# Kernel tuning notes

Measured on AMD Instinct MI355X. Metric: run time of the kernel, lower is better.

Reference implementation:

```python
import jax, jax.numpy as jnp
import numpy as np

N_USER, N_ITEM, N_BUNDLE = 200000, 100000, 50000
EMBED_DIM = 128
B, L = 8192, 100  # batch of bundles, max items per bundle


def setup_inputs() -> dict:
    key = jax.random.key(0)
    ks = jax.random.split(key, 12)
    d, d2 = EMBED_DIM, 2 * EMBED_DIM
    x_u = jax.random.randint(ks[0], (B,), 0, N_USER)
    x_b = jax.random.randint(ks[1], (B,), 0, N_BUNDLE)
    items = jax.random.randint(ks[2], (B, L), 0, N_ITEM)
    # ragged bundle sizes in [10, L]; padded+masked form of the CSR gather
    lengths = jax.random.randint(ks[3], (B,), 10, L + 1)
    mask = jnp.arange(L)[None, :] < lengths[:, None]  # [B, L] bool
    return {
        "x_u": x_u,
        "x_b": x_b,
        "items": items,
        "mask": mask,
        "emb_u": jax.random.normal(ks[4], (N_USER, d), jnp.float32) * 0.1,
        "emb_i": jax.random.normal(ks[5], (N_ITEM, d), jnp.float32) * 0.1,
        "emb_b": jax.random.normal(ks[6], (N_BUNDLE, d), jnp.float32) * 0.1,
        "A": jax.random.normal(ks[7], (N_ITEM, d), jnp.float32) * 0.1,
        "fc1_w": jax.random.normal(ks[8], (d2, d2), jnp.float32) / np.sqrt(d2),
        "fc1_b": jnp.zeros((d2,), jnp.float32),
        "fc2_w": jax.random.normal(ks[9], (d2, d2), jnp.float32) / np.sqrt(d2),
        "fc2_b": jnp.zeros((d2,), jnp.float32),
        "out_w": jax.random.normal(ks[10], (1, d2), jnp.float32) / np.sqrt(d2),
        "out_b": jnp.zeros((1,), jnp.float32),
    }


def reference(x_u, x_b, items, mask, emb_u, emb_i, emb_b, A,
              fc1_w, fc1_b, fc2_w, fc2_b, out_w, out_b):
    # DAM.forward_bundle with the attention() per-bundle loop vectorized
    h_u = emb_u[x_u]                       # [B, d]
    h_b = emb_b[x_b]                       # [B, d]
    item_e = emb_i[items]                  # [B, L, d] ragged gather (padded)
    a_e = A[items]                         # [B, L, d]
    # w = softmax_l( sum_d e_u * A[item] ) per bundle, over valid items only
    scores = jnp.einsum('bd,bld->bl', h_u, a_e)
    scores = jnp.where(mask, scores, -jnp.inf)
    w = jax.nn.softmax(scores, axis=1)     # [B, L]
    h_x = jnp.einsum('bl,bld->bd', w, item_e)
    h = jnp.concatenate([h_u, h_b + h_x], axis=1)   # [B, 2d]
    h = jax.nn.leaky_relu(h @ fc1_w.T + fc1_b)
    h = jax.nn.leaky_relu(h @ fc2_w.T + fc2_b)
    return h @ out_w.T + out_b             # [B, 1]
```

## Files before the change

### kernel.cpp

```cpp
#include <hip/hip_runtime.h>
#include <hip/hip_bf16.h>

#define D   128
#define D2  256
#define H1P 272

typedef short bf16x8 __attribute__((ext_vector_type(8)));
typedef float f32x4  __attribute__((ext_vector_type(4)));

__device__ __forceinline__ float bf2f(unsigned short u) {
    return __uint_as_float(((unsigned int)u) << 16);
}
__device__ __forceinline__ float bflo(unsigned int p) { return __uint_as_float(p << 16); }
__device__ __forceinline__ float bfhi(unsigned int p) { return __uint_as_float(p & 0xffff0000u); }
__device__ __forceinline__ unsigned short f2bf(float f) {
    __hip_bfloat16 h = __float2bfloat16(f);
    return *(unsigned short*)&h;
}

template<bool BF>
__device__ __forceinline__ float ld1(const void* p, size_t i) {
    if constexpr (BF) return bf2f(((const unsigned short*)p)[i]);
    else              return ((const float*)p)[i];
}

template<bool BF>
__device__ __forceinline__ void load8f(const void* p, size_t elem_off, float* r) {
    if constexpr (BF) {
        uint4 v = *(const uint4*)((const unsigned short*)p + elem_off);
        r[0]=bflo(v.x); r[1]=bfhi(v.x); r[2]=bflo(v.y); r[3]=bfhi(v.y);
        r[4]=bflo(v.z); r[5]=bfhi(v.z); r[6]=bflo(v.w); r[7]=bfhi(v.w);
    } else {
        const float4* q = (const float4*)((const float*)p + elem_off);
        float4 a = q[0], b = q[1];
        r[0]=a.x; r[1]=a.y; r[2]=a.z; r[3]=a.w;
        r[4]=b.x; r[5]=b.y; r[6]=b.z; r[7]=b.w;
    }
}

__device__ __forceinline__ int probe_bf16(const unsigned int* probe, int lane) {
    int cnt = 0;
    #pragma unroll
    for (int i = 0; i < 4; ++i) {
        unsigned int e = (probe[lane + 64 * i] >> 7) & 0xffu;
        cnt += (e >= 90 && e < 130) ? 1 : 0;
    }
    #pragma unroll
    for (int o = 32; o; o >>= 1) cnt += __shfl_xor(cnt, o);
    return cnt;
}

template<bool BF>
__device__ __forceinline__ void attn_body(
    const int* __restrict__ x_u, const int* __restrict__ x_b,
    const int* __restrict__ items, const void* __restrict__ mask, int mmode,
    const void* __restrict__ emb_u, const void* __restrict__ emb_i,
    const void* __restrict__ emb_b, const void* __restrict__ Aw,
    unsigned short* __restrict__ h_out, int L,
    float* hu_s, float* sc_s, float* w_s, int* it_s,
    int* cnt_s, float* reds_s, float (*part_s)[132])
{
    const int b  = blockIdx.x;
    const int t  = threadIdx.x;
    const int wv = t >> 6, ln = t & 63;

    const int xu = x_u[b], xb = x_b[b];
    float hu = 0.f;
    if (t < D) { hu = ld1<BF>(emb_u, (size_t)xu * D + t); hu_s[t] = hu; }

    bool valid = false;
    if (t < L && t < 128) {
        const size_t mi = (size_t)b * L + t;
        it_s[t] = items[mi];
        if (mmode == 0)      valid = ((const int*)mask)[mi] != 0;
        else if (mmode == 1) valid = ((const unsigned char*)mask)[mi] != 0;
        else                 valid = ((const unsigned short*)mask)[mi] != 0;
    }
    unsigned long long bm = __ballot(valid);
    if (ln == 0) cnt_s[wv] = __popcll(bm);
    __syncthreads();
    const int len = cnt_s[0] + cnt_s[1] + cnt_s[2] + cnt_s[3];

    const int item = t >> 1, half = t & 1;
    if (item < len) {
        float acc = 0.f, r[8];
        const size_t base = (size_t)it_s[item] * D + half * 64;
        const float4* hu4 = (const float4*)hu_s + half * 16;
        #pragma unroll
        for (int c = 0; c < 8; ++c) {
            load8f<BF>(Aw, base + 8 * c, r);
            float4 ha = hu4[2 * c], hb2 = hu4[2 * c + 1];
            acc += ha.x * r[0] + ha.y * r[1] + ha.z * r[2] + ha.w * r[3]
                 + hb2.x * r[4] + hb2.y * r[5] + hb2.z * r[6] + hb2.w * r[7];
        }
        acc += __shfl_xor(acc, 1);
        if (half == 0) sc_s[item] = acc;
    }
    if (t >= len && t < 128) it_s[t] = it_s[0];
    __syncthreads();

    const int g = t >> 4, m16 = t & 15;

    uint4 pre0[4], pre1[4];
    if constexpr (BF) {
        const unsigned short* EI = (const unsigned short*)emb_i;
        #pragma unroll
        for (int i = 0; i < 4; ++i) {
            pre0[i] = *(const uint4*)(EI + (size_t)it_s[32 * i + g]      * D + 8 * m16);
            pre1[i] = *(const uint4*)(EI + (size_t)it_s[32 * i + 16 + g] * D + 8 * m16);
        }
    }

    const float e = (t < len) ? __expf(sc_s[t]) : 0.f;
    if (t < 128) w_s[t] = e;
    float sm = e;
    #pragma unroll
    for (int o = 32; o; o >>= 1) sm += __shfl_xor(sm, o);
    if (ln == 0) reds_s[wv] = sm;
    __syncthreads();
    sm = reds_s[0] + reds_s[1] + reds_s[2] + reds_s[3];
    const float inv = (sm > 0.f) ? 1.f / sm : 0.f;

    float acc8[8];
    #pragma unroll
    for (int k = 0; k < 8; ++k) acc8[k] = 0.f;
    if constexpr (BF) {
        #pragma unroll
        for (int i = 0; i < 4; ++i) {
            const float w0 = w_s[32 * i + g], w1 = w_s[32 * i + 16 + g];
            const uint4 p0 = pre0[i], p1 = pre1[i];
            acc8[0] += w0 * bflo(p0.x) + w1 * bflo(p1.x);
            acc8[1] += w0 * bfhi(p0.x) + w1 * bfhi(p1.x);
            acc8[2] += w0 * bflo(p0.y) + w1 * bflo(p1.y);
            acc8[3] += w0 * bfhi(p0.y) + w1 * bfhi(p1.y);
            acc8[4] += w0 * bflo(p0.z) + w1 * bflo(p1.z);
            acc8[5] += w0 * bfhi(p0.z) + w1 * bfhi(p1.z);
            acc8[6] += w0 * bflo(p0.w) + w1 * bflo(p1.w);
            acc8[7] += w0 * bfhi(p0.w) + w1 * bfhi(p1.w);
        }
    } else {
        const int nit = (len + 31) & ~31;
        for (int i = 0; i < nit; i += 32) {
            const float w0 = w_s[i + g], w1 = w_s[i + 16 + g];
            float r0[8], r1[8];
            load8f<false>(emb_i, (size_t)it_s[i + g] * D + 8 * m16, r0);
            load8f<false>(emb_i, (size_t)it_s[i + 16 + g] * D + 8 * m16, r1);
            #pragma unroll
            for (int k = 0; k < 8; ++k) acc8[k] += w0 * r0[k] + w1 * r1[k];
        }
    }
    f32x4 v0 = {acc8[0] * inv, acc8[1] * inv, acc8[2] * inv, acc8[3] * inv};
    f32x4 v1 = {acc8[4] * inv, acc8[5] * inv, acc8[6] * inv, acc8[7] * inv};
    *(f32x4*)&part_s[g][8 * m16]     = v0;
    *(f32x4*)&part_s[g][8 * m16 + 4] = v1;
    __syncthreads();

    if (t < D) {
        float hx = 0.f;
        #pragma unroll
        for (int gg = 0; gg < 16; ++gg) hx += part_s[gg][t];
        const float hbv = ld1<BF>(emb_b, (size_t)xb * D + t);
        h_out[(size_t)b * D2 + t]     = f2bf(hu);
        h_out[(size_t)b * D2 + D + t] = f2bf(hbv + hx);
    }
}

__global__ __launch_bounds__(256) void attn_kernel(
    const int* x_u, const int* x_b, const int* items, const void* mask,
    const void* emb_u, const void* emb_i, const void* emb_b, const void* A,
    unsigned short* h_out, int L)
{
    __shared__ float hu_s[D];
    __shared__ float sc_s[128];
    __shared__ float w_s[128];
    __shared__ int   it_s[128];
    __shared__ int   cnt_s[4];
    __shared__ float reds_s[4];
    __shared__ float part_s[16][132];
    __shared__ int   flag_s[2];

    const int t = threadIdx.x;
    if (t < 64) {
        int cnt = probe_bf16((const unsigned int*)emb_u, t);
        if (t == 0) {
            const unsigned char* mb = (const unsigned char*)mask;
            flag_s[0] = (cnt >= 128) ? 1 : 0;
            flag_s[1] = (mb[1] == 0) ? 0 : ((mb[0] == 1) ? 1 : 2);
        }
    }
    __syncthreads();

    if (flag_s[0]) attn_body<true >(x_u, x_b, items, mask, flag_s[1], emb_u, emb_i, emb_b, A,
                                    h_out, L, hu_s, sc_s, w_s, it_s, cnt_s, reds_s, part_s);
    else           attn_body<false>(x_u, x_b, items, mask, flag_s[1], emb_u, emb_i, emb_b, A,
                                    h_out, L, hu_s, sc_s, w_s, it_s, cnt_s, reds_s, part_s);
}

template<bool BF>
__device__ __forceinline__ bf16x8 load_w8(const void* W, size_t off) {
    if constexpr (BF) {
        return *(const bf16x8*)((const unsigned short*)W + off);
    } else {
        const float* p = (const float*)W + off;
        float4 a = *(const float4*)p;
        float4 b = *(const float4*)(p + 4);
        bf16x8 r;
        r[0] = (short)f2bf(a.x); r[1] = (short)f2bf(a.y);
        r[2] = (short)f2bf(a.z); r[3] = (short)f2bf(a.w);
        r[4] = (short)f2bf(b.x); r[5] = (short)f2bf(b.y);
        r[6] = (short)f2bf(b.z); r[7] = (short)f2bf(b.w);
        return r;
    }
}

template<bool BF>
__device__ __forceinline__ void mlp_body(
    const unsigned short* __restrict__ X,
    const void* __restrict__ fc1_w, const void* __restrict__ fc1_b,
    const void* __restrict__ fc2_w, const void* __restrict__ fc2_b,
    const void* __restrict__ out_w, const void* __restrict__ out_b,
    void* __restrict__ out,
    unsigned short* h1_s, float (*po_s)[16])
{
    const int tid  = threadIdx.x;
    const int wave = tid >> 6;
    const int lane = tid & 63;
    const int l16  = lane & 15;
    const int quad = lane >> 4;
    const int mt   = blockIdx.x * 16;

    bf16x8 afrag[8];
    const size_t abase = (size_t)(mt + l16) * D2 + quad * 8;
    #pragma unroll
    for (int kc = 0; kc < 8; ++kc)
        afrag[kc] = *(const bf16x8*)(X + abase + kc * 32);

    #pragma unroll
    for (int jj = 0; jj < 4; ++jj) {
        const int jt = wave * 4 + jj;
        const size_t bbase = (size_t)(jt * 16 + l16) * D2 + quad * 8;
        f32x4 acc = {0.f, 0.f, 0.f, 0.f};
        #pragma unroll
        for (int kc = 0; kc < 8; ++kc) {
            bf16x8 bfrag = load_w8<BF>(fc1_w, bbase + kc * 32);
            acc = __builtin_amdgcn_mfma_f32_16x16x32_bf16(afrag[kc], bfrag, acc, 0, 0, 0);
        }
        const int j  = jt * 16 + l16;
        const float bj = ld1<BF>(fc1_b, j);
        #pragma unroll
        for (int r = 0; r < 4; ++r) {
            float v = acc[r] + bj;
            v = v > 0.f ? v : 0.01f * v;
            h1_s[(quad * 4 + r) * H1P + j] = f2bf(v);
        }
    }
    __syncthreads();

    bf16x8 afrag2[8];
    #pragma unroll
    for (int kc = 0; kc < 8; ++kc)
        afrag2[kc] = *(const bf16x8*)&h1_s[l16 * H1P + quad * 8 + kc * 32];

    float po[4] = {0.f, 0.f, 0.f, 0.f};
    #pragma unroll
    for (int jj = 0; jj < 4; ++jj) {
        const int jt = wave * 4 + jj;
        const size_t bbase = (size_t)(jt * 16 + l16) * D2 + quad * 8;
        f32x4 acc = {0.f, 0.f, 0.f, 0.f};
        #pragma unroll
        for (int kc = 0; kc < 8; ++kc) {
            bf16x8 bfrag = load_w8<BF>(fc2_w, bbase + kc * 32);
            acc = __builtin_amdgcn_mfma_f32_16x16x32_bf16(afrag2[kc], bfrag, acc, 0, 0, 0);
        }
        const int j  = jt * 16 + l16;
        const float bj = ld1<BF>(fc2_b, j);
        const float wj = ld1<BF>(out_w, j);
        #pragma unroll
        for (int r = 0; r < 4; ++r) {
            float v = acc[r] + bj;
            v = v > 0.f ? v : 0.01f * v;
            po[r] += v * wj;
        }
    }
    #pragma unroll
    for (int r = 0; r < 4; ++r) {
        #pragma unroll
        for (int o = 1; o < 16; o <<= 1) po[r] += __shfl_xor(po[r], o);
    }
    if (l16 == 0) {
        #pragma unroll
        for (int r = 0; r < 4; ++r) po_s[wave][quad * 4 + r] = po[r];
    }
    __syncthreads();

    if (tid < 16) {
        const float v = po_s[0][tid] + po_s[1][tid] + po_s[2][tid] + po_s[3][tid]
                      + ld1<BF>(out_b, 0);
        if constexpr (BF) ((unsigned short*)out)[mt + tid] = f2bf(v);
        else              ((float*)out)[mt + tid] = v;
    }
}

__global__ __launch_bounds__(256) void mlp_kernel(
    const unsigned short* X,
    const void* fc1_w, const void* fc1_b, const void* fc2_w, const void* fc2_b,
    const void* out_w, const void* out_b, void* out, const void* probe)
{
    __shared__ unsigned short h1_s[16 * H1P];
    __shared__ float po_s[4][16];
    __shared__ int flag_s;

    const int t = threadIdx.x;
    if (t < 64) {
        int cnt = probe_bf16((const unsigned int*)probe, t);
        if (t == 0) flag_s = (cnt >= 128) ? 1 : 0;
    }
    __syncthreads();

    if (flag_s) mlp_body<true >(X, fc1_w, fc1_b, fc2_w, fc2_b, out_w, out_b, out, h1_s, po_s);
    else        mlp_body<false>(X, fc1_w, fc1_b, fc2_w, fc2_b, out_w, out_b, out, h1_s, po_s);
}

extern "C" void kernel_launch(void* const* d_in, const int* in_sizes, int n_in,
                              void* d_out, int out_size, void* d_ws, size_t ws_size,
                              hipStream_t stream) {
    const int*  x_u   = (const int*)d_in[0];
    const int*  x_b   = (const int*)d_in[1];
    const int*  items = (const int*)d_in[2];
    const void* mask  = d_in[3];
    const void* emb_u = d_in[4];
    const void* emb_i = d_in[5];
    const void* emb_b = d_in[6];
    const void* A     = d_in[7];
    const void* fc1_w = d_in[8];
    const void* fc1_b = d_in[9];
    const void* fc2_w = d_in[10];
    const void* fc2_b = d_in[11];
    const void* out_w = d_in[12];
    const void* out_b = d_in[13];

    const int B = in_sizes[0];
    const int L = in_sizes[2] / B;

    unsigned short* h = (unsigned short*)d_ws;

    attn_kernel<<<B, 256, 0, stream>>>(x_u, x_b, items, mask,
                                       emb_u, emb_i, emb_b, A, h, L);
    mlp_kernel<<<B / 16, 256, 0, stream>>>(h, fc1_w, fc1_b, fc2_w, fc2_b,
                                           out_w, out_b, d_out, emb_u);
}
```

Measured before the change: 330.9 us.

## Drop barriers in attention kernel, fuse exp into scores, hoist item prefetch

Each wavefront now runs the dtype probe itself instead of one wave probing and broadcasting through shared memory behind a barrier, in both kernels. The score stage applies exp directly and writes weights, which removes the score buffer and one barrier. The emb_i prefetch is issued before the score dot products and clamped to valid items, limited to 96 rows with a conditional tail. The aim is fewer block-wide syncs and earlier gather latency, at the cost of redundant probe work per wave and more live registers during the score loop.

```diff
diff --git a/kernel.cpp b/kernel.cpp
--- a/kernel.cpp
+++ b/kernel.cpp
@@ -38,7 +38,8 @@
     }
 }
 
-__device__ __forceinline__ int probe_bf16(const unsigned int* probe, int lane) {
+__device__ __forceinline__ bool probe_is_bf16(const unsigned int* probe) {
+    const int lane = threadIdx.x & 63;
     int cnt = 0;
     #pragma unroll
     for (int i = 0; i < 4; ++i) {
@@ -47,7 +48,7 @@
     }
     #pragma unroll
     for (int o = 32; o; o >>= 1) cnt += __shfl_xor(cnt, o);
-    return cnt;
+    return cnt >= 128;
 }
 
 template<bool BF>
@@ -57,8 +58,8 @@
     const void* __restrict__ emb_u, const void* __restrict__ emb_i,
     const void* __restrict__ emb_b, const void* __restrict__ Aw,
     unsigned short* __restrict__ h_out, int L,
-    float* hu_s, float* sc_s, float* w_s, int* it_s,
-    int* cnt_s, float* reds_s, float (*part_s)[132])
+    float* hu_s, float* w_s, int* it_s, int* cnt_s, float* reds_s,
+    float (*part_s)[132])
 {
     const int b  = blockIdx.x;
     const int t  = threadIdx.x;
@@ -69,19 +70,38 @@
     if (t < D) { hu = ld1<BF>(emb_u, (size_t)xu * D + t); hu_s[t] = hu; }
 
     bool valid = false;
-    if (t < L && t < 128) {
-        const size_t mi = (size_t)b * L + t;
-        it_s[t] = items[mi];
-        if (mmode == 0)      valid = ((const int*)mask)[mi] != 0;
-        else if (mmode == 1) valid = ((const unsigned char*)mask)[mi] != 0;
-        else                 valid = ((const unsigned short*)mask)[mi] != 0;
+    if (t < 128) {
+        const int tc = (t < L) ? t : (L - 1);
+        it_s[t] = items[(size_t)b * L + tc];
+        if (t < L) {
+            const size_t mi = (size_t)b * L + t;
+            if (mmode == 0)      valid = ((const int*)mask)[mi] != 0;
+            else if (mmode == 1) valid = ((const unsigned char*)mask)[mi] != 0;
+            else                 valid = ((const unsigned short*)mask)[mi] != 0;
+        }
     }
     unsigned long long bm = __ballot(valid);
     if (ln == 0) cnt_s[wv] = __popcll(bm);
     __syncthreads();
     const int len = cnt_s[0] + cnt_s[1] + cnt_s[2] + cnt_s[3];
 
+    const int g = t >> 4, m16 = t & 15;
+
+    uint4 pre0[3], pre1[3];
+    if constexpr (BF) {
+        const unsigned short* EI = (const unsigned short*)emb_i;
+        #pragma unroll
+        for (int i = 0; i < 3; ++i) {
+            const int l0 = 32 * i + g, l1 = 32 * i + 16 + g;
+            const int i0 = (l0 < len) ? it_s[l0] : it_s[0];
+            const int i1 = (l1 < len) ? it_s[l1] : it_s[0];
+            pre0[i] = *(const uint4*)(EI + (size_t)i0 * D + 8 * m16);
+            pre1[i] = *(const uint4*)(EI + (size_t)i1 * D + 8 * m16);
+        }
+    }
+
     const int item = t >> 1, half = t & 1;
+    float e = 0.f;
     if (item < len) {
         float acc = 0.f, r[8];
         const size_t base = (size_t)it_s[item] * D + half * 64;
@@ -94,31 +114,15 @@
                  + hb2.x * r[4] + hb2.y * r[5] + hb2.z * r[6] + hb2.w * r[7];
         }
         acc += __shfl_xor(acc, 1);
-        if (half == 0) sc_s[item] = acc;
-    }
-    if (t >= len && t < 128) it_s[t] = it_s[0];
-    __syncthreads();
-
-    const int g = t >> 4, m16 = t & 15;
-
-    uint4 pre0[4], pre1[4];
-    if constexpr (BF) {
-        const unsigned short* EI = (const unsigned short*)emb_i;
-        #pragma unroll
-        for (int i = 0; i < 4; ++i) {
-            pre0[i] = *(const uint4*)(EI + (size_t)it_s[32 * i + g]      * D + 8 * m16);
-            pre1[i] = *(const uint4*)(EI + (size_t)it_s[32 * i + 16 + g] * D + 8 * m16);
-        }
-    }
-
-    const float e = (t < len) ? __expf(sc_s[t]) : 0.f;
-    if (t < 128) w_s[t] = e;
-    float sm = e;
-    #pragma unroll
-    for (int o = 32; o; o >>= 1) sm += __shfl_xor(sm, o);
-    if (ln == 0) reds_s[wv] = sm;
-    __syncthreads();
-    sm = reds_s[0] + reds_s[1] + reds_s[2] + reds_s[3];
+        e = __expf(acc);
+    }
+    if (half == 0) w_s[item] = e;
+    float es = (half == 0) ? e : 0.f;
+    #pragma unroll
+    for (int o = 32; o; o >>= 1) es += __shfl_xor(es, o);
+    if (ln == 0) reds_s[wv] = es;
+    __syncthreads();
+    const float sm  = reds_s[0] + reds_s[1] + reds_s[2] + reds_s[3];
     const float inv = (sm > 0.f) ? 1.f / sm : 0.f;
 
     float acc8[8];
@@ -126,7 +130,7 @@
     for (int k = 0; k < 8; ++k) acc8[k] = 0.f;
     if constexpr (BF) {
         #pragma unroll
-        for (int i = 0; i < 4; ++i) {
+        for (int i = 0; i < 3; ++i) {
             const float w0 = w_s[32 * i + g], w1 = w_s[32 * i + 16 + g];
             const uint4 p0 = pre0[i], p1 = pre1[i];
             acc8[0] += w0 * bflo(p0.x) + w1 * bflo(p1.x);
@@ -138,13 +142,27 @@
             acc8[6] += w0 * bflo(p0.w) + w1 * bflo(p1.w);
             acc8[7] += w0 * bfhi(p0.w) + w1 * bfhi(p1.w);
         }
+        if (len > 96) {
+            const int l0 = 96 + g;
+            const int i0 = (l0 < len) ? it_s[l0] : it_s[0];
+            const float w0 = w_s[l0];
+            const uint4 p0 = *(const uint4*)((const unsigned short*)emb_i
+                                             + (size_t)i0 * D + 8 * m16);
+            acc8[0] += w0 * bflo(p0.x); acc8[1] += w0 * bfhi(p0.x);
+            acc8[2] += w0 * bflo(p0.y); acc8[3] += w0 * bfhi(p0.y);
+            acc8[4] += w0 * bflo(p0.z); acc8[5] += w0 * bfhi(p0.z);
+            acc8[6] += w0 * bflo(p0.w); acc8[7] += w0 * bfhi(p0.w);
+        }
     } else {
         const int nit = (len + 31) & ~31;
         for (int i = 0; i < nit; i += 32) {
-            const float w0 = w_s[i + g], w1 = w_s[i + 16 + g];
+            const int l0 = i + g, l1 = i + 16 + g;
+            const int i0 = (l0 < len) ? it_s[l0] : it_s[0];
+            const int i1 = (l1 < len) ? it_s[l1] : it_s[0];
+            const float w0 = w_s[l0], w1 = w_s[l1];
             float r0[8], r1[8];
-            load8f<false>(emb_i, (size_t)it_s[i + g] * D + 8 * m16, r0);
-            load8f<false>(emb_i, (size_t)it_s[i + 16 + g] * D + 8 * m16, r1);
+            load8f<false>(emb_i, (size_t)i0 * D + 8 * m16, r0);
+            load8f<false>(emb_i, (size_t)i1 * D + 8 * m16, r1);
             #pragma unroll
             for (int k = 0; k < 8; ++k) acc8[k] += w0 * r0[k] + w1 * r1[k];
         }
@@ -171,29 +189,20 @@
     unsigned short* h_out, int L)
 {
     __shared__ float hu_s[D];
-    __shared__ float sc_s[128];
     __shared__ float w_s[128];
     __shared__ int   it_s[128];
     __shared__ int   cnt_s[4];
     __shared__ float reds_s[4];
     __shared__ float part_s[16][132];
-    __shared__ int   flag_s[2];
-
-    const int t = threadIdx.x;
-    if (t < 64) {
-        int cnt = probe_bf16((const unsigned int*)emb_u, t);
-        if (t == 0) {
-            const unsigned char* mb = (const unsigned char*)mask;
-            flag_s[0] = (cnt >= 128) ? 1 : 0;
-            flag_s[1] = (mb[1] == 0) ? 0 : ((mb[0] == 1) ? 1 : 2);
-        }
-    }
-    __syncthreads();
-
-    if (flag_s[0]) attn_body<true >(x_u, x_b, items, mask, flag_s[1], emb_u, emb_i, emb_b, A,
-                                    h_out, L, hu_s, sc_s, w_s, it_s, cnt_s, reds_s, part_s);
-    else           attn_body<false>(x_u, x_b, items, mask, flag_s[1], emb_u, emb_i, emb_b, A,
-                                    h_out, L, hu_s, sc_s, w_s, it_s, cnt_s, reds_s, part_s);
+
+    const bool bf = probe_is_bf16((const unsigned int*)emb_u);
+    const unsigned char* mb = (const unsigned char*)mask;
+    const int mm = (mb[1] == 0) ? 0 : ((mb[0] == 1) ? 1 : 2);
+
+    if (bf) attn_body<true >(x_u, x_b, items, mask, mm, emb_u, emb_i, emb_b, A,
+                             h_out, L, hu_s, w_s, it_s, cnt_s, reds_s, part_s);
+    else    attn_body<false>(x_u, x_b, items, mask, mm, emb_u, emb_i, emb_b, A,
+                             h_out, L, hu_s, w_s, it_s, cnt_s, reds_s, part_s);
 }
 
 template<bool BF>
@@ -308,17 +317,10 @@
 {
     __shared__ unsigned short h1_s[16 * H1P];
     __shared__ float po_s[4][16];
-    __shared__ int flag_s;
-
-    const int t = threadIdx.x;
-    if (t < 64) {
-        int cnt = probe_bf16((const unsigned int*)probe, t);
-        if (t == 0) flag_s = (cnt >= 128) ? 1 : 0;
-    }
-    __syncthreads();
-
-    if (flag_s) mlp_body<true >(X, fc1_w, fc1_b, fc2_w, fc2_b, out_w, out_b, out, h1_s, po_s);
-    else        mlp_body<false>(X, fc1_w, fc1_b, fc2_w, fc2_b, out_w, out_b, out, h1_s, po_s);
+
+    const bool bf = probe_is_bf16((const unsigned int*)probe);
+    if (bf) mlp_body<true >(X, fc1_w, fc1_b, fc2_w, fc2_b, out_w, out_b, out, h1_s, po_s);
+    else    mlp_body<false>(X, fc1_w, fc1_b, fc2_w, fc2_b, out_w, out_b, out, h1_s, po_s);
 }
 
 extern "C" void kernel_launch(void* const* d_in, const int* in_sizes, int n_in,
```

Measured after the change: 320.7 us. 1.03x faster.
